# Kernel tuning notes

Hardware: AMD Instinct MI355X
Metric: run time of the kernel (lower is better)

Reference implementation:

```python
import jax, jax.numpy as jnp
import numpy as np

RCR = 5.2
RCA = 3.5
NUM_SPECIES = 4


def _triu_index(ns):
    i, j = np.triu_indices(ns)
    t = np.zeros((ns, ns), dtype=np.int32)
    idx = np.arange(len(i), dtype=np.int32)
    t[i, j] = idx
    t[j, i] = idx
    return jnp.asarray(t)


TRIU_INDEX = _triu_index(NUM_SPECIES)


def setup_inputs() -> dict:
    key = jax.random.key(0)
    k1, k2 = jax.random.split(key)
    B, N = 128, 32
    coordinates = jax.random.uniform(k1, (B, N, 3), dtype=jnp.float32) * 6.0  # ~6A box
    species = jax.random.randint(k2, (B, N), 0, NUM_SPECIES, dtype=jnp.int32)
    EtaR = jnp.array([16.0], dtype=jnp.float32)
    ShfR = jnp.linspace(0.9, 4.93125, 16, dtype=jnp.float32)
    EtaA = jnp.array([8.0], dtype=jnp.float32)
    Zeta = jnp.array([32.0], dtype=jnp.float32)
    ShfA = jnp.linspace(0.9, 2.85, 4, dtype=jnp.float32)
    ShfZ = jnp.linspace(0.19634954, 2.94524311, 8, dtype=jnp.float32)
    return {"coordinates": coordinates, "EtaR": EtaR, "ShfR": ShfR, "EtaA": EtaA,
            "Zeta": Zeta, "ShfA": ShfA, "ShfZ": ShfZ, "species": species}


def _aev(coordinates, EtaR, ShfR, EtaA, Zeta, ShfA, ShfZ, species):
    B, N, _ = coordinates.shape
    valid = species >= 0
    sp = jnp.clip(species, 0, NUM_SPECIES - 1)
    # pairwise vectors v[b,i,j] = r_j - r_i  (vector from central atom i to j)
    vec = coordinates[:, None, :, :] - coordinates[:, :, None, :]  # (B,N,N,3)
    d2 = jnp.sum(vec * vec, axis=-1)
    eye = jnp.eye(N, dtype=bool)
    d = jnp.sqrt(jnp.where(d2 > 0, d2, 1.0))  # safe sqrt, diag masked below
    pair_ok = valid[:, :, None] & valid[:, None, :] & (~eye)[None]

    # ---- radial AEV: eq (3) ----
    mR = pair_ok & (d <= RCR)
    fcR = 0.5 * jnp.cos(d * (np.pi / RCR)) + 0.5
    # (B,N,N,E,S): 0.25*exp(-EtaR*(d-ShfR)^2)*fc
    rt = 0.25 * jnp.exp(-EtaR[:, None] * (d[..., None, None] - ShfR[None, :]) ** 2) * fcR[..., None, None]
    rt = rt * mR[..., None, None].astype(rt.dtype)
    rt = rt.reshape(B, N, N, -1)  # (B,N,N,16)
    oh = jax.nn.one_hot(species, NUM_SPECIES, dtype=rt.dtype)  # (B,N,4); -1 -> all-zero
    radial = jnp.einsum('bijr,bjs->bisr', rt, oh).reshape(B, N, -1)  # (B,N,64)

    # ---- angular AEV: eq (4), summed over unordered neighbor pairs ----
    mA = pair_ok & (d <= RCA)
    tmask = mA[:, :, :, None] & mA[:, :, None, :] & (~eye)[None, None, :, :]  # (B,N,N,N), j!=k
    dij = d[:, :, :, None]
    dik = d[:, :, None, :]
    cosang = jnp.einsum('bijd,bikd->bijk', vec, vec) / jnp.maximum(dij * dik, 1e-10)
    ang = jnp.arccos(0.95 * cosang)  # (B,N,N,N)
    fcA = 0.5 * jnp.cos(d * (np.pi / RCA)) + 0.5
    fprod = fcA[:, :, :, None] * fcA[:, :, None, :]
    dmean = (dij + dik) * 0.5
    A, Z, P, T = EtaA.shape[0], Zeta.shape[0], ShfA.shape[0], ShfZ.shape[0]
    # factor1: ((1+cos(theta-ShfZ))/2)^Zeta -> (B,N,N,N,Z,T)
    f1 = ((1.0 + jnp.cos(ang[..., None, None] - ShfZ[None, :])) * 0.5) ** Zeta[:, None]
    # factor2: exp(-EtaA*((dij+dik)/2 - ShfA)^2) -> (B,N,N,N,A,P)
    f2 = jnp.exp(-EtaA[:, None] * (dmean[..., None, None] - ShfA[None, :]) ** 2)
    # (B,N,N,N,A,Z,P,T) then flatten sublength in (EtaA,Zeta,ShfA,ShfZ) order
    term = 2.0 * f1[..., None, :, None, :] * f2[..., :, None, :, None] \
        * (fprod * tmask.astype(f1.dtype))[..., None, None, None, None]
    term = term.reshape(B, N, N, N, A * Z * P * T)  # (B,N,N,N,32)
    npairs = NUM_SPECIES * (NUM_SPECIES + 1) // 2
    pidx = TRIU_INDEX[sp[:, :, None], sp[:, None, :]]  # (B,N,N) species-pair bucket
    poh = jax.nn.one_hot(pidx, npairs, dtype=term.dtype)  # (B,N,N,10)
    # 0.5: ordered (j,k) double-counts the symmetric unordered pairs
    angular = 0.5 * jnp.einsum('bijkf,bjkp->bipf', term, poh)
    angular = angular.reshape(B, N, -1)  # (B,N,320)

    return jnp.concatenate([radial, angular], axis=-1)  # (B,N,384)


def reference(coordinates, EtaR, ShfR, EtaA, Zeta, ShfA, ShfZ, species):
    return _aev(coordinates, EtaR, ShfR, EtaA, Zeta, ShfA, ShfZ, species)
```

## Files before the change

kernel.cpp:

```cpp
#include <hip/hip_runtime.h>
#include <hip/hip_fp16.h>
#include <math.h>

#define NATOM   32
#define NSP     4
#define NCLS    10
#define NSHFR   16
#define NSHFA   4
#define NSHFZ   8
#define FEAT_ANG (NSHFA * NSHFZ)
#define OUT_PER_ATOM (NSP * NSHFR + NCLS * FEAT_ANG)
#define MAXP    465

#define RCR_F 5.2f
#define RCA_F 3.5f
#define PI_F  3.14159265358979323846f

__device__ __forceinline__ int tri(int n) { return (n * (n - 1)) >> 1; }

template <bool FAST>
__device__ __forceinline__ void angular_accum(
    const float2* __restrict__ pc_cs, const __half* __restrict__ pc_eh,
    int s0, int e0, int p, float ct, float st, float zt, float& acc)
{
#pragma unroll 2
    for (int pp = s0; pp < e0; ++pp) {
        const float2 cs = pc_cs[pp];
        const float  ee = __half2float(pc_eh[pp * 4 + p]);
        const float u = fmaf(cs.x, ct, fmaf(cs.y, st, 0.5f));
        float f1;
        if (FAST) {
            const float u2 = u * u, u4 = u2 * u2, u8 = u4 * u4, u16 = u8 * u8;
            f1 = u16 * u16;
        } else {
            f1 = __powf(fmaxf(u, 0.f), zt);
        }
        acc = fmaf(f1, ee, acc);
    }
}

__global__ __launch_bounds__(64) void aev_kernel(
    const float* __restrict__ coords,
    const float* __restrict__ etaR,
    const float* __restrict__ shfR,
    const float* __restrict__ etaA,
    const float* __restrict__ zeta,
    const float* __restrict__ shfA,
    const float* __restrict__ shfZ,
    const int*   __restrict__ species,
    float* __restrict__ out)
{
    const int atom = blockIdx.x;
    const int b    = atom >> 5;
    const int i    = atom & 31;
    const int tid  = threadIdx.x;

    __shared__ float sco[NATOM * 3];
    __shared__ float sd_o[NATOM], sfcR_o[NATOM];
    __shared__ int   ssp_o[NATOM];
    __shared__ float nvx[NATOM], nvy[NATOM], nvz[NATOM];
    __shared__ float nd[NATOM], nfa[NATOM];
    __shared__ int   s_off[NCLS + 1];
    __shared__ float2 pc_cs[MAXP];
    __shared__ __align__(8) __half pc_eh[MAXP * 4];

    for (int t = tid; t < NATOM * 3; t += 64) sco[t] = coords[b * (NATOM * 3) + t];
    int spj = -1, spi = -1;
    if (tid < NATOM) {
        spj = species[b * NATOM + tid];
        spi = species[b * NATOM + i];
    }
    __syncthreads();

    bool  act = false;
    int   sp  = 0;
    float vx = 0.f, vy = 0.f, vz = 0.f, d = 0.f, fcA = 0.f;
    if (tid < NATOM) {
        const int j = tid;
        const float cx = sco[i * 3 + 0], cy = sco[i * 3 + 1], cz = sco[i * 3 + 2];
        vx = sco[j * 3 + 0] - cx;
        vy = sco[j * 3 + 1] - cy;
        vz = sco[j * 3 + 2] - cz;
        const float d2 = vx * vx + vy * vy + vz * vz;
        d = sqrtf(d2 > 0.f ? d2 : 1.f);
        const bool ok = (j != i) && (spj >= 0) && (spi >= 0);
        fcA = (ok && d <= RCA_F) ? (0.5f * __cosf(d * (PI_F / RCA_F)) + 0.5f) : 0.f;
        const float fcR = (ok && d <= RCR_F) ? (0.5f * __cosf(d * (PI_F / RCR_F)) + 0.5f) : 0.f;
        sp = spj < 0 ? 0 : (spj > (NSP - 1) ? (NSP - 1) : spj);
        sd_o[j] = d; sfcR_o[j] = fcR; ssp_o[j] = sp;
        act = fcA > 0.f;
    }

    const unsigned long long m0 = __ballot(act && sp == 0);
    const unsigned long long m1 = __ballot(act && sp == 1);
    const unsigned long long m2 = __ballot(act && sp == 2);
    const unsigned long long m3 = __ballot(act && sp == 3);
    const int n0 = (int)__popcll(m0), n1 = (int)__popcll(m1);
    const int n2 = (int)__popcll(m2), n3 = (int)__popcll(m3);
    const int B1 = n0, B2 = n0 + n1, B3 = n0 + n1 + n2;
    const int nn = B3 + n3;

    if (act) {
        const unsigned long long lt = (1ull << tid) - 1ull;
        int pos;
        if      (sp == 0) pos =      (int)__popcll(m0 & lt);
        else if (sp == 1) pos = B1 + (int)__popcll(m1 & lt);
        else if (sp == 2) pos = B2 + (int)__popcll(m2 & lt);
        else              pos = B3 + (int)__popcll(m3 & lt);
        nvx[pos] = vx; nvy[pos] = vy; nvz[pos] = vz;
        nd[pos] = d; nfa[pos] = fcA;
    }

    const int c0 = tri(n0), c1 = n0 * n1, c2 = n0 * n2, c3 = n0 * n3;
    const int c4 = tri(n1), c5 = n1 * n2, c6 = n1 * n3;
    const int c7 = tri(n2), c8 = n2 * n3, c9 = tri(n3);
    const int np = c0 + c1 + c2 + c3 + c4 + c5 + c6 + c7 + c8 + c9;
    {
        int v = 0;
        v += (0 < tid) ? c0 : 0;  v += (1 < tid) ? c1 : 0;
        v += (2 < tid) ? c2 : 0;  v += (3 < tid) ? c3 : 0;
        v += (4 < tid) ? c4 : 0;  v += (5 < tid) ? c5 : 0;
        v += (6 < tid) ? c6 : 0;  v += (7 < tid) ? c7 : 0;
        v += (8 < tid) ? c8 : 0;  v += (9 < tid) ? c9 : 0;
        if (tid <= NCLS) s_off[tid] = v;
    }
    __syncthreads();

    const long obase = (long)atom * OUT_PER_ATOM;

    {
        const int r  = tid & 15;
        const int jg = tid >> 4;
        const float shf = shfR[r];
        const float eta = etaR[0];
        float a0 = 0.f, a1 = 0.f, a2 = 0.f, a3 = 0.f;
        for (int j = jg; j < NATOM; j += 4) {
            const float fc = sfcR_o[j];
            if (fc > 0.f) {
                const float dd = sd_o[j] - shf;
                const float v = 0.25f * __expf(-eta * dd * dd) * fc;
                const int s = ssp_o[j];
                a0 += (s == 0) ? v : 0.f;
                a1 += (s == 1) ? v : 0.f;
                a2 += (s == 2) ? v : 0.f;
                a3 += (s == 3) ? v : 0.f;
            }
        }
        a0 += __shfl_xor(a0, 16); a0 += __shfl_xor(a0, 32);
        a1 += __shfl_xor(a1, 16); a1 += __shfl_xor(a1, 32);
        a2 += __shfl_xor(a2, 16); a2 += __shfl_xor(a2, 32);
        a3 += __shfl_xor(a3, 16); a3 += __shfl_xor(a3, 32);
        if (tid < 16) {
            out[obase + 0 * NSHFR + r] = a0;
            out[obase + 1 * NSHFR + r] = a1;
            out[obase + 2 * NSHFR + r] = a2;
            out[obase + 3 * NSHFR + r] = a3;
        }
    }

    const float eA  = etaA[0];
    const float sa0 = shfA[0], sa1 = shfA[1], sa2 = shfA[2], sa3 = shfA[3];
    for (int base = 0; base < np; base += 64) {
        const int p = base + tid;
        if (p < np) {
            const int tnn = 2 * nn - 1;
            int a = (int)(((float)tnn - sqrtf((float)(tnn * tnn - 8 * p))) * 0.5f);
            if (a < 0) a = 0;
            int Sa = a * (nn - 1) - tri(a);
            if (Sa > p) { --a; Sa = a * (nn - 1) - tri(a); }
            else {
                const int San = (a + 1) * (nn - 1) - tri(a + 1);
                if (San <= p) { ++a; Sa = San; }
            }
            const int bb = a + 1 + (p - Sa);
            const int sa = (a  >= B1) + (a  >= B2) + (a  >= B3);
            const int sb = (bb >= B1) + (bb >= B2) + (bb >= B3);
            const int cls = sa * NSP - tri(sa) + (sb - sa);
            const int Bs  = (sa == 0) ? 0 : ((sa == 1) ? B1 : ((sa == 2) ? B2 : B3));
            const int Bt  = (sb == 0) ? 0 : ((sb == 1) ? B1 : ((sb == 2) ? B2 : B3));
            const int ns_ = (sa == 0) ? n0 : ((sa == 1) ? n1 : ((sa == 2) ? n2 : n3));
            const int nt_ = (sb == 0) ? n0 : ((sb == 1) ? n1 : ((sb == 2) ? n2 : n3));
            int lidx;
            if (sa == sb) {
                const int aa = a - Bs, bb2 = bb - Bs;
                lidx = aa * (ns_ - 1) - tri(aa) + (bb2 - aa - 1);
            } else {
                lidx = (a - Bs) * nt_ + (bb - Bt);
            }
            const int pos = s_off[cls] + lidx;
            const float da = nd[a], db = nd[bb];
            const float dot = nvx[a] * nvx[bb] + nvy[a] * nvy[bb] + nvz[a] * nvz[bb];
            const float cv = 0.95f * dot * __builtin_amdgcn_rcpf(fmaxf(da * db, 1e-10f));
            const float sv = __builtin_amdgcn_sqrtf(fmaxf(1.f - cv * cv, 0.f));
            const float dm = 0.5f * (da + db);
            const float fac = 2.f * nfa[a] * nfa[bb];
            const float d0 = dm - sa0, d1 = dm - sa1, d2 = dm - sa2, d3 = dm - sa3;
            const float e0 = fac * __expf(-eA * d0 * d0);
            const float e1 = fac * __expf(-eA * d1 * d1);
            const float e2 = fac * __expf(-eA * d2 * d2);
            const float e3 = fac * __expf(-eA * d3 * d3);
            pc_cs[pos] = make_float2(0.5f * cv, 0.5f * sv);
            __half2* dst = reinterpret_cast<__half2*>(pc_eh + pos * 4);
            dst[0] = __floats2half2_rn(e0, e1);
            dst[1] = __floats2half2_rn(e2, e3);
        }
    }
    __syncthreads();

    {
        const int f = tid & 31;
        const int p = f >> 3;
        const int t = f & 7;
        const int half = tid >> 5;
        float st, ct;
        __sincosf(shfZ[t], &st, &ct);
        const float zt = zeta[0];
        float* oang = out + obase + NSP * NSHFR;

        if (zt == 32.0f) {
#pragma unroll
            for (int qi = 0; qi < NCLS / 2; ++qi) {
                const int q = qi * 2 + half;
                const int s0 = s_off[q], e0 = s_off[q + 1];
                float acc = 0.f;
                angular_accum<true>(pc_cs, pc_eh, s0, e0, p, ct, st, zt, acc);
                oang[q * FEAT_ANG + f] = acc;
            }
        } else {
#pragma unroll
            for (int qi = 0; qi < NCLS / 2; ++qi) {
                const int q = qi * 2 + half;
                const int s0 = s_off[q], e0 = s_off[q + 1];
                float acc = 0.f;
                angular_accum<false>(pc_cs, pc_eh, s0, e0, p, ct, st, zt, acc);
                oang[q * FEAT_ANG + f] = acc;
            }
        }
    }
}

extern "C" void kernel_launch(void* const* d_in, const int* in_sizes, int n_in,
                              void* d_out, int out_size, void* d_ws, size_t ws_size,
                              hipStream_t stream) {
    const float* coords  = (const float*)d_in[0];
    const float* etaR    = (const float*)d_in[1];
    const float* shfR    = (const float*)d_in[2];
    const float* etaA    = (const float*)d_in[3];
    const float* zeta    = (const float*)d_in[4];
    const float* shfA    = (const float*)d_in[5];
    const float* shfZ    = (const float*)d_in[6];
    const int*   species = (const int*)d_in[7];
    float* out = (float*)d_out;

    const int B = in_sizes[0] / (NATOM * 3);
    aev_kernel<<<B * NATOM, 64, 0, stream>>>(coords, etaR, shfR, etaA, zeta,
                                             shfA, shfZ, species, out);
}
```

Baseline: 86.47 us.

## Pack shared-memory pair and neighbor data into float4 and restructure radial loop

Merges the separate cos/sin float2 array and the half-precision exp array into a single float4 record per pair, so the angular accumulation does one 16-byte LDS load per pair instead of two loads. Neighbor vectors and distances are packed the same way, and radial inputs go into float4 records. The radial stage now gives each thread one (species, shift) output and loops over all 32 neighbors, removing the cross-lane shuffle reductions and predicated stores. The cost is more exp evaluations in the radial loop, since non-cutoff and other-species neighbors are no longer skipped, plus a per-pair select to extract the right half value.

```diff
diff --git a/kernel.cpp b/kernel.cpp
--- a/kernel.cpp
+++ b/kernel.cpp
@@ -19,24 +19,35 @@
 __device__ __forceinline__ int tri(int n) { return (n * (n - 1)) >> 1; }
 
 template <bool FAST>
+__device__ __forceinline__ float pair_term(float4 r, int p, float ct, float st, float zt)
+{
+    const float u = fmaf(r.x, ct, fmaf(r.y, st, 0.5f));
+    float f1;
+    if (FAST) {
+        const float u2 = u * u, u4 = u2 * u2, u8 = u4 * u4, u16 = u8 * u8;
+        f1 = u16 * u16;
+    } else {
+        f1 = __powf(fmaxf(u, 0.f), zt);
+    }
+    const unsigned ez = (p & 2) ? __float_as_uint(r.w) : __float_as_uint(r.z);
+    const __half2 hh = *reinterpret_cast<const __half2*>(&ez);
+    const float e = (p & 1) ? __high2float(hh) : __low2float(hh);
+    return f1 * e;
+}
+
+template <bool FAST>
 __device__ __forceinline__ void angular_accum(
-    const float2* __restrict__ pc_cs, const __half* __restrict__ pc_eh,
-    int s0, int e0, int p, float ct, float st, float zt, float& acc)
+    const float4* __restrict__ pc, int s0, int e0, int p,
+    float ct, float st, float zt, float& acc)
 {
-#pragma unroll 2
-    for (int pp = s0; pp < e0; ++pp) {
-        const float2 cs = pc_cs[pp];
-        const float  ee = __half2float(pc_eh[pp * 4 + p]);
-        const float u = fmaf(cs.x, ct, fmaf(cs.y, st, 0.5f));
-        float f1;
-        if (FAST) {
-            const float u2 = u * u, u4 = u2 * u2, u8 = u4 * u4, u16 = u8 * u8;
-            f1 = u16 * u16;
-        } else {
-            f1 = __powf(fmaxf(u, 0.f), zt);
-        }
-        acc = fmaf(f1, ee, acc);
-    }
+    int pp = s0;
+    for (; pp + 2 <= e0; pp += 2) {
+        const float4 r0 = pc[pp];
+        const float4 r1 = pc[pp + 1];
+        acc += pair_term<FAST>(r0, p, ct, st, zt);
+        acc += pair_term<FAST>(r1, p, ct, st, zt);
+    }
+    if (pp < e0) acc += pair_term<FAST>(pc[pp], p, ct, st, zt);
 }
 
 __global__ __launch_bounds__(64) void aev_kernel(
@@ -56,13 +67,11 @@
     const int tid  = threadIdx.x;
 
     __shared__ float sco[NATOM * 3];
-    __shared__ float sd_o[NATOM], sfcR_o[NATOM];
-    __shared__ int   ssp_o[NATOM];
-    __shared__ float nvx[NATOM], nvy[NATOM], nvz[NATOM];
-    __shared__ float nd[NATOM], nfa[NATOM];
+    __shared__ __align__(16) float4 srad[NATOM];
+    __shared__ __align__(16) float4 nvd[NATOM];
+    __shared__ float nfa[NATOM];
     __shared__ int   s_off[NCLS + 1];
-    __shared__ float2 pc_cs[MAXP];
-    __shared__ __align__(8) __half pc_eh[MAXP * 4];
+    __shared__ __align__(16) float4 pc[MAXP];
 
     for (int t = tid; t < NATOM * 3; t += 64) sco[t] = coords[b * (NATOM * 3) + t];
     int spj = -1, spi = -1;
@@ -87,7 +96,7 @@
         fcA = (ok && d <= RCA_F) ? (0.5f * __cosf(d * (PI_F / RCA_F)) + 0.5f) : 0.f;
         const float fcR = (ok && d <= RCR_F) ? (0.5f * __cosf(d * (PI_F / RCR_F)) + 0.5f) : 0.f;
         sp = spj < 0 ? 0 : (spj > (NSP - 1) ? (NSP - 1) : spj);
-        sd_o[j] = d; sfcR_o[j] = fcR; ssp_o[j] = sp;
+        srad[j] = make_float4(d, fcR, (float)sp, 0.f);
         act = fcA > 0.f;
     }
 
@@ -107,8 +116,8 @@
         else if (sp == 1) pos = B1 + (int)__popcll(m1 & lt);
         else if (sp == 2) pos = B2 + (int)__popcll(m2 & lt);
         else              pos = B3 + (int)__popcll(m3 & lt);
-        nvx[pos] = vx; nvy[pos] = vy; nvz[pos] = vz;
-        nd[pos] = d; nfa[pos] = fcA;
+        nvd[pos] = make_float4(vx, vy, vz, d);
+        nfa[pos] = fcA;
     }
 
     const int c0 = tri(n0), c1 = n0 * n1, c2 = n0 * n2, c3 = n0 * n3;
@@ -129,33 +138,20 @@
     const long obase = (long)atom * OUT_PER_ATOM;
 
     {
+        const int s  = tid >> 4;
         const int r  = tid & 15;
-        const int jg = tid >> 4;
+        const float sf  = (float)s;
         const float shf = shfR[r];
         const float eta = etaR[0];
-        float a0 = 0.f, a1 = 0.f, a2 = 0.f, a3 = 0.f;
-        for (int j = jg; j < NATOM; j += 4) {
-            const float fc = sfcR_o[j];
-            if (fc > 0.f) {
-                const float dd = sd_o[j] - shf;
-                const float v = 0.25f * __expf(-eta * dd * dd) * fc;
-                const int s = ssp_o[j];
-                a0 += (s == 0) ? v : 0.f;
-                a1 += (s == 1) ? v : 0.f;
-                a2 += (s == 2) ? v : 0.f;
-                a3 += (s == 3) ? v : 0.f;
-            }
+        float acc = 0.f;
+#pragma unroll 4
+        for (int j = 0; j < NATOM; ++j) {
+            const float4 rd = srad[j];
+            const float dd = rd.x - shf;
+            const float v  = __expf(-eta * dd * dd) * rd.y;
+            acc += (rd.z == sf) ? v : 0.f;
         }
-        a0 += __shfl_xor(a0, 16); a0 += __shfl_xor(a0, 32);
-        a1 += __shfl_xor(a1, 16); a1 += __shfl_xor(a1, 32);
-        a2 += __shfl_xor(a2, 16); a2 += __shfl_xor(a2, 32);
-        a3 += __shfl_xor(a3, 16); a3 += __shfl_xor(a3, 32);
-        if (tid < 16) {
-            out[obase + 0 * NSHFR + r] = a0;
-            out[obase + 1 * NSHFR + r] = a1;
-            out[obase + 2 * NSHFR + r] = a2;
-            out[obase + 3 * NSHFR + r] = a3;
-        }
+        out[obase + tid] = 0.25f * acc;
     }
 
     const float eA  = etaA[0];
@@ -188,8 +184,10 @@
                 lidx = (a - Bs) * nt_ + (bb - Bt);
             }
             const int pos = s_off[cls] + lidx;
-            const float da = nd[a], db = nd[bb];
-            const float dot = nvx[a] * nvx[bb] + nvy[a] * nvy[bb] + nvz[a] * nvz[bb];
+            const float4 va = nvd[a];
+            const float4 vb = nvd[bb];
+            const float da = va.w, db = vb.w;
+            const float dot = va.x * vb.x + va.y * vb.y + va.z * vb.z;
             const float cv = 0.95f * dot * __builtin_amdgcn_rcpf(fmaxf(da * db, 1e-10f));
             const float sv = __builtin_amdgcn_sqrtf(fmaxf(1.f - cv * cv, 0.f));
             const float dm = 0.5f * (da + db);
@@ -199,10 +197,11 @@
             const float e1 = fac * __expf(-eA * d1 * d1);
             const float e2 = fac * __expf(-eA * d2 * d2);
             const float e3 = fac * __expf(-eA * d3 * d3);
-            pc_cs[pos] = make_float2(0.5f * cv, 0.5f * sv);
-            __half2* dst = reinterpret_cast<__half2*>(pc_eh + pos * 4);
-            dst[0] = __floats2half2_rn(e0, e1);
-            dst[1] = __floats2half2_rn(e2, e3);
+            const __half2 h01 = __floats2half2_rn(e0, e1);
+            const __half2 h23 = __floats2half2_rn(e2, e3);
+            pc[pos] = make_float4(0.5f * cv, 0.5f * sv,
+                                  __uint_as_float(*reinterpret_cast<const unsigned*>(&h01)),
+                                  __uint_as_float(*reinterpret_cast<const unsigned*>(&h23)));
         }
     }
     __syncthreads();
@@ -221,18 +220,16 @@
 #pragma unroll
             for (int qi = 0; qi < NCLS / 2; ++qi) {
                 const int q = qi * 2 + half;
-                const int s0 = s_off[q], e0 = s_off[q + 1];
                 float acc = 0.f;
-                angular_accum<true>(pc_cs, pc_eh, s0, e0, p, ct, st, zt, acc);
+                angular_accum<true>(pc, s_off[q], s_off[q + 1], p, ct, st, zt, acc);
                 oang[q * FEAT_ANG + f] = acc;
             }
         } else {
 #pragma unroll
             for (int qi = 0; qi < NCLS / 2; ++qi) {
                 const int q = qi * 2 + half;
-                const int s0 = s_off[q], e0 = s_off[q + 1];
                 float acc = 0.f;
-                angular_accum<false>(pc_cs, pc_eh, s0, e0, p, ct, st, zt, acc);
+                angular_accum<false>(pc, s_off[q], s_off[q + 1], p, ct, st, zt, acc);
                 oang[q * FEAT_ANG + f] = acc;
             }
         }
```

Result: slower. 89.35 us (+3.3%).
